# Optimization experiments

Measured on AMD Instinct MI355X. Metric: run time of the kernel, lower is better.

The kernel has to match this reference:

```python
import jax, jax.numpy as jnp
import numpy as np

V, H, O = 256, 1024, 1024   # input_dim, hidden_dim, output_dim
B, T = 64, 512


def setup_inputs() -> dict:
    key = jax.random.key(0)
    ks = jax.random.split(key, 12)
    s = 1.0 / np.sqrt(H)  # torch nn.RNN / nn.Linear init range
    u = lambda k, shp: jax.random.uniform(k, shp, jnp.float32, -s, s)
    return {
        "x": jax.random.randint(ks[0], (B, T), 0, V),
        "W_ih_f": u(ks[1], (H, V)), "W_hh_f": u(ks[2], (H, H)),
        "b_ih_f": u(ks[3], (H,)),   "b_hh_f": u(ks[4], (H,)),
        "W_ih_b": u(ks[5], (H, V)), "W_hh_b": u(ks[6], (H, H)),
        "b_ih_b": u(ks[7], (H,)),   "b_hh_b": u(ks[8], (H,)),
        "W_fc": u(ks[9], (O, 2 * H)), "b_fc": u(ks[10], (O,)),
    }


def _scan_rnn(xW, W_hh):
    # xW: [T,B,H] precomputed input contribution (x W_ih^T + b_ih + b_hh)
    def step(h, xw):
        h = jnp.tanh(xw + h @ W_hh.T)
        return h, h
    h0 = jnp.zeros((xW.shape[1], W_hh.shape[0]), xW.dtype)
    _, hs = jax.lax.scan(step, h0, xW)
    return hs  # [T,B,H]


def reference(x, W_ih_f, W_hh_f, b_ih_f, b_hh_f,
              W_ih_b, W_hh_b, b_ih_b, b_hh_b, W_fc, b_fc):
    # one_hot(x, V) @ W_ih^T  ==  W_ih.T[x]  (gather; same math, no dense one-hot)
    xW_f = W_ih_f.T[x] + b_ih_f + b_hh_f          # [B,T,H]
    xW_b = W_ih_b.T[x] + b_ih_b + b_hh_b          # [B,T,H]
    hf = _scan_rnn(jnp.swapaxes(xW_f, 0, 1), W_hh_f)            # [T,B,H]
    hb = _scan_rnn(jnp.swapaxes(xW_b, 0, 1)[::-1], W_hh_b)[::-1]  # [T,B,H]
    out = jnp.swapaxes(jnp.concatenate([hf, hb], axis=-1), 0, 1)  # [B,T,2H]
    return out @ W_fc.T + b_fc                    # [B,T,O]
```

## Files before the change

kernel.cpp:

```cpp
#include <hip/hip_runtime.h>
#include <math.h>

#define B_ 64
#define T_ 512
#define H_ 1024
#define V_ 256
#define O_ 1024
#define KFC 2048

typedef short bf16x8 __attribute__((ext_vector_type(8)));
typedef _Float16 f16x8 __attribute__((ext_vector_type(8)));
typedef float f32x4 __attribute__((ext_vector_type(4)));
typedef int   i32x4 __attribute__((ext_vector_type(4)));
typedef unsigned long long u64x2 __attribute__((ext_vector_type(2)));

#define FLIP64 0x8000800080008000ULL

#define OFF_TABLE_F 0
#define OFF_TABLE_B 1048576
#define OFF_XT      2097152
#define OFF_WHH     2228224
#define OFF_WFC     6422528
#define OFF_HSF     10616832
#define OFF_HSB     77725696

__device__ __forceinline__ float fast_tanh(float zz) {
  float e = __expf(2.0f * zz);
  return 1.0f - 2.0f * __builtin_amdgcn_rcpf(e + 1.0f);
}

__global__ void prep_kernel(const int* __restrict__ x,
    const float* __restrict__ WihF, const float* __restrict__ WhhF,
    const float* __restrict__ bihF, const float* __restrict__ bhhF,
    const float* __restrict__ WihB, const float* __restrict__ WhhB,
    const float* __restrict__ bihB, const float* __restrict__ bhhB,
    const float* __restrict__ Wfc,
    float* __restrict__ tableF, float* __restrict__ tableB,
    int* __restrict__ xT, short* __restrict__ whhpack,
    short* __restrict__ wfcpack, unsigned long long* __restrict__ hsz)
{
  const long NT1 = 524288, NT2 = 32768, NT3 = 2097152, NT4 = 2097152;
  const long NT5 = 16777216;
  const long total = NT1 + NT2 + NT3 + NT4 + NT5;
  for (long i = (long)blockIdx.x * blockDim.x + threadIdx.x; i < total;
       i += (long)gridDim.x * blockDim.x) {
    long j = i;
    if (j < NT1) {
      int d = (int)(j >> 18);
      int r = (int)(j & 262143);
      int v = r >> 10, h = r & 1023;
      const float* Wih = d ? WihB : WihF;
      const float* bi  = d ? bihB : bihF;
      const float* bh  = d ? bhhB : bhhF;
      (d ? tableB : tableF)[r] = Wih[h * V_ + v] + bi[h] + bh[h];
      continue;
    }
    j -= NT1;
    if (j < NT2) {
      int t = (int)(j >> 6), bb = (int)(j & 63);
      xT[j] = x[bb * T_ + t];
      continue;
    }
    j -= NT2;
    if (j < NT3) {
      int d = (int)(j >> 20);
      int r = (int)(j & 1048575);
      int jj = r & 7;
      int lanei = (r >> 3) & 63;
      int kt = (r >> 9) & 31;
      int cti = (r >> 14) & 3;
      int csi = (r >> 16) & 15;
      int c = csi * 64 + cti * 16 + (lanei & 15);
      int k = kt * 32 + (lanei >> 4) * 8 + jj;
      float w = (d ? WhhB : WhhF)[c * H_ + k];
      _Float16 wh = (_Float16)w;
      whhpack[j] = __builtin_bit_cast(short, wh);
      continue;
    }
    j -= NT3;
    if (j < NT4) {
      int jj = (int)(j & 7);
      int lanei = (int)((j >> 3) & 63);
      int nti = (int)((j >> 9) & 3);
      int k32 = (int)((j >> 11) & 63);
      int obi = (int)(j >> 17);
      int o = obi * 64 + nti * 16 + (lanei & 15);
      int k = k32 * 32 + (lanei >> 4) * 8 + jj;
      _Float16 wf = (_Float16)Wfc[(long)o * KFC + k];
      wfcpack[j] = __builtin_bit_cast(short, wf);
      continue;
    }
    j -= NT4;
    hsz[j] = 0ULL;
    continue;
  }
}

__global__ __launch_bounds__(256, 1)
void rnn_kernel(const int* __restrict__ xT,
                const float* __restrict__ tableF, const float* __restrict__ tableB,
                const short* __restrict__ whhpack,
                unsigned long long* __restrict__ hsfF,
                unsigned long long* __restrict__ hsfB)
{
  extern __shared__ char lds[];
  char* ldsH = lds;
  const int tid = threadIdx.x;
  const int wg = blockIdx.x;
  const int dir = wg >> 6;
  const int bt = (wg >> 4) & 3;
  const int cs = wg & 15;
  const int lane = tid & 63;
  const int ct = tid >> 6;
  const int row = bt * 16 + (lane & 15);
  const int c4 = cs * 64 + ct * 16 + (lane >> 4) * 4;
  const float* table = dir ? tableB : tableF;
  unsigned long long* hsx = dir ? hsfB : hsfF;
  const int pub_off = bt * 4096 + (c4 >> 5) * 128 + ((c4 >> 2) & 1) * 64 +
                      (lane & 15) + ((c4 >> 3) & 3) * 16;

  f16x8 Wreg[32];
  {
    const i32x4* wsrc = (const i32x4*)whhpack + (size_t)(dir * 16 + cs) * 8192;
    #pragma unroll
    for (int kt = 0; kt < 32; ++kt)
      Wreg[kt] = __builtin_bit_cast(f16x8, wsrc[(ct * 32 + kt) * 64 + lane]);
  }

  const f32x4 zv = {0.f, 0.f, 0.f, 0.f};

  {
    int t0 = dir ? 511 : 0;
    int v = xT[t0 * 64 + row];
    f32x4 xwv = *(const f32x4*)(table + v * 1024 + c4);
    unsigned long long hx = 0;
    #pragma unroll
    for (int r = 0; r < 4; ++r) {
      float h = fast_tanh(xwv[r]);
      union { _Float16 f; unsigned short u; } cv; cv.f = (_Float16)h;
      unsigned short u = (cv.u == 0x8000u) ? 0u : cv.u;
      hx |= (unsigned long long)(u ^ 0x8000u) << (16 * r);
    }
    __hip_atomic_store(hsx + (size_t)t0 * 16384 + pub_off, hx,
                       __ATOMIC_RELAXED, __HIP_MEMORY_SCOPE_AGENT);
  }

#define LDX(p) __hip_atomic_load((p), __ATOMIC_RELAXED, __HIP_MEMORY_SCOPE_AGENT)

  for (int s = 1; s < 512; ++s) {
    const int t = dir ? (511 - s) : s;
    const int tprev = dir ? (t + 1) : (t - 1);
    int v = xT[t * 64 + row];
    f32x4 xwv = *(const f32x4*)(table + v * 1024 + c4);

    const unsigned long long* sp =
        hsx + (size_t)tprev * 16384 + bt * 4096 + tid * 2;
    unsigned long long a0[4], b0[4], a1[4], b1[4];
    #pragma unroll
    for (int i = 0; i < 4; ++i) {
      a0[i] = LDX(sp + i * 512);
      b0[i] = LDX(sp + i * 512 + 1);
    }
    #pragma unroll
    for (int i = 0; i < 4; ++i) {
      a1[i] = LDX(sp + (4 + i) * 512);
      b1[i] = LDX(sp + (4 + i) * 512 + 1);
    }

    for (;;) {
      int miss = 0;
      #pragma unroll
      for (int i = 0; i < 4; ++i)
        miss |= (a0[i] == 0ULL) | (b0[i] == 0ULL);
      if (!__ballot(miss)) break;
      __builtin_amdgcn_s_sleep(1);
      #pragma unroll
      for (int i = 0; i < 4; ++i) {
        a0[i] = LDX(sp + i * 512);
        b0[i] = LDX(sp + i * 512 + 1);
      }
    }
    #pragma unroll
    for (int jj = 0; jj < 4; ++jj) {
      u64x2 w; w[0] = a0[jj] ^ FLIP64; w[1] = b0[jj] ^ FLIP64;
      *(u64x2*)(ldsH + jj * 4096 + tid * 16) = w;
    }
    asm volatile("s_waitcnt lgkmcnt(0)" ::: "memory");
    __builtin_amdgcn_s_barrier();
    asm volatile("" ::: "memory");

    f32x4 acc4[4] = {zv, zv, zv, zv};
    #pragma unroll
    for (int kt = 0; kt < 16; ++kt) {
      u64x2 bv;
      bv[0] = *(const unsigned long long*)(ldsH + (kt * 128 + lane) * 8);
      bv[1] = *(const unsigned long long*)(ldsH + (kt * 128 + 64 + lane) * 8);
      f16x8 bf = __builtin_bit_cast(f16x8, bv);
      acc4[kt & 3] =
          __builtin_amdgcn_mfma_f32_16x16x32_f16(Wreg[kt], bf, acc4[kt & 3], 0, 0, 0);
    }

    for (;;) {
      int miss = 0;
      #pragma unroll
      for (int i = 0; i < 4; ++i)
        miss |= (a1[i] == 0ULL) | (b1[i] == 0ULL);
      if (!__ballot(miss)) break;
      __builtin_amdgcn_s_sleep(1);
      #pragma unroll
      for (int i = 0; i < 4; ++i) {
        a1[i] = LDX(sp + (4 + i) * 512);
        b1[i] = LDX(sp + (4 + i) * 512 + 1);
      }
    }
    #pragma unroll
    for (int jj = 0; jj < 4; ++jj) {
      u64x2 w; w[0] = a1[jj] ^ FLIP64; w[1] = b1[jj] ^ FLIP64;
      *(u64x2*)(ldsH + (4 + jj) * 4096 + tid * 16) = w;
    }
    asm volatile("s_waitcnt lgkmcnt(0)" ::: "memory");
    __builtin_amdgcn_s_barrier();
    asm volatile("" ::: "memory");

    #pragma unroll
    for (int kt = 16; kt < 32; ++kt) {
      u64x2 bv;
      bv[0] = *(const unsigned long long*)(ldsH + (kt * 128 + lane) * 8);
      bv[1] = *(const unsigned long long*)(ldsH + (kt * 128 + 64 + lane) * 8);
      f16x8 bf = __builtin_bit_cast(f16x8, bv);
      acc4[kt & 3] =
          __builtin_amdgcn_mfma_f32_16x16x32_f16(Wreg[kt], bf, acc4[kt & 3], 0, 0, 0);
    }

    f32x4 accs = (acc4[0] + acc4[1]) + (acc4[2] + acc4[3]);
    unsigned long long hx = 0;
    #pragma unroll
    for (int r = 0; r < 4; ++r) {
      float h = fast_tanh(accs[r] + xwv[r]);
      union { _Float16 f; unsigned short u; } cv; cv.f = (_Float16)h;
      unsigned short u = (cv.u == 0x8000u) ? 0u : cv.u;
      hx |= (unsigned long long)(u ^ 0x8000u) << (16 * r);
    }
    __hip_atomic_store(hsx + (size_t)t * 16384 + pub_off, hx,
                       __ATOMIC_RELAXED, __HIP_MEMORY_SCOPE_AGENT);
  }
#undef LDX
}

__global__ __launch_bounds__(256, 2)
void fc_kernel(const unsigned long long* __restrict__ hsfF,
               const unsigned long long* __restrict__ hsfB,
               const short* __restrict__ wfcpack, const float* __restrict__ bfc,
               float* __restrict__ out)
{
  __shared__ unsigned long long Alds[4096];
  __shared__ short Blds[4096];
  const int tid = threadIdx.x;
  const int lane = tid & 63;
  const int w = tid >> 6;
  const int t = blockIdx.x * 4 + w;
  const int ob = blockIdx.y;
  const int btl = lane >> 4;
  const int li = lane & 15;

  const i32x4 flip32 = {(int)0x80008000, (int)0x80008000,
                        (int)0x80008000, (int)0x80008000};
  f32x4 z = {0.f, 0.f, 0.f, 0.f};
  f32x4 acc[4][4] = {{z, z, z, z}, {z, z, z, z}, {z, z, z, z}, {z, z, z, z}};
  unsigned long long* Aw = &Alds[w * 1024];

  for (int kc = 0; kc < 32; ++kc) {
    {
      const unsigned long long* src =
          (kc < 16 ? hsfF : hsfB) + (size_t)t * 16384;
      int kt0 = (kc & 15) * 2;
      const unsigned long long* ap = src + btl * 4096 + kt0 * 128 + li * 8;
      #pragma unroll
      for (int rr = 0; rr < 2; ++rr) {
        i32x4 q0 = *(const i32x4*)(ap + rr * 128) ^ flip32;
        i32x4 q1 = *(const i32x4*)(ap + rr * 128 + 2) ^ flip32;
        i32x4 q2 = *(const i32x4*)(ap + rr * 128 + 4) ^ flip32;
        i32x4 q3 = *(const i32x4*)(ap + rr * 128 + 6) ^ flip32;
        unsigned long long* dst = &Aw[(btl * 2 + rr) * 128 + li * 8];
        *(i32x4*)(dst) = q0;
        *(i32x4*)(dst + 2) = q1;
        *(i32x4*)(dst + 4) = q2;
        *(i32x4*)(dst + 6) = q3;
      }
    }
    {
      const i32x4* src = (const i32x4*)(wfcpack + ((size_t)ob * 64 + kc * 2) * 2048);
      i32x4* dst = (i32x4*)Blds;
      dst[tid] = src[tid];
      dst[tid + 256] = src[tid + 256];
    }
    __syncthreads();
    #pragma unroll
    for (int k2 = 0; k2 < 2; ++k2) {
      f16x8 afr[4];
      #pragma unroll
      for (int mi = 0; mi < 4; ++mi) {
        u64x2 av;
        av[0] = Aw[(mi * 2 + k2) * 128 + lane];
        av[1] = Aw[(mi * 2 + k2) * 128 + 64 + lane];
        afr[mi] = __builtin_bit_cast(f16x8, av);
      }
      #pragma unroll
      for (int ni = 0; ni < 4; ++ni) {
        f16x8 bfr = *(const f16x8*)((const char*)Blds + ((k2 * 4 + ni) * 64 + lane) * 16);
        #pragma unroll
        for (int mi = 0; mi < 4; ++mi)
          acc[mi][ni] = __builtin_amdgcn_mfma_f32_16x16x32_f16(afr[mi], bfr, acc[mi][ni], 0, 0, 0);
      }
    }
    __syncthreads();
  }
  #pragma unroll
  for (int mi = 0; mi < 4; ++mi) {
    #pragma unroll
    for (int ni = 0; ni < 4; ++ni) {
      int o = ob * 64 + ni * 16 + (lane & 15);
      float bias = bfc[o];
      #pragma unroll
      for (int r = 0; r < 4; ++r) {
        int b = mi * 16 + (lane >> 4) * 4 + r;
        out[(size_t)(b * 512 + t) * O_ + o] = acc[mi][ni][r] + bias;
      }
    }
  }
}

extern "C" void kernel_launch(void* const* d_in, const int* in_sizes, int n_in,
                              void* d_out, int out_size, void* d_ws, size_t ws_size,
                              hipStream_t stream) {
  const int* x = (const int*)d_in[0];
  const float* WihF = (const float*)d_in[1];
  const float* WhhF = (const float*)d_in[2];
  const float* bihF = (const float*)d_in[3];
  const float* bhhF = (const float*)d_in[4];
  const float* WihB = (const float*)d_in[5];
  const float* WhhB = (const float*)d_in[6];
  const float* bihB = (const float*)d_in[7];
  const float* bhhB = (const float*)d_in[8];
  const float* Wfc  = (const float*)d_in[9];
  const float* bfc  = (const float*)d_in[10];
  float* out = (float*)d_out;
  char* ws = (char*)d_ws;

  float* tableF = (float*)(ws + OFF_TABLE_F);
  float* tableB = (float*)(ws + OFF_TABLE_B);
  int* xT = (int*)(ws + OFF_XT);
  short* whhpack = (short*)(ws + OFF_WHH);
  short* wfcpack = (short*)(ws + OFF_WFC);
  unsigned long long* hsfF = (unsigned long long*)(ws + OFF_HSF);
  unsigned long long* hsfB = (unsigned long long*)(ws + OFF_HSB);

  hipFuncSetAttribute((const void*)rnn_kernel,
                      hipFuncAttributeMaxDynamicSharedMemorySize, 32768);

  prep_kernel<<<dim3(2048), dim3(256), 0, stream>>>(
      x, WihF, WhhF, bihF, bhhF, WihB, WhhB, bihB, bhhB, Wfc,
      tableF, tableB, xT, whhpack, wfcpack, hsfF);
  rnn_kernel<<<dim3(128), dim3(256), 32768, stream>>>(
      xT, tableF, tableB, whhpack, hsfF, hsfB);
  fc_kernel<<<dim3(128, 16), dim3(256), 0, stream>>>(
      hsfF, hsfB, wfcpack, bfc, out);
}
```

Baseline: 1.553 ms.

## Halve RNN workgroups, each computing two column tiles with streamed weights

The recurrent kernel now launches 64 workgroups instead of 128, and each wave computes two 16-column tiles per step instead of one. The W_hh fragments are no longer held in registers. They are reloaded from global memory (likely served from cache) inside every timestep's MFMA loop. This means fewer workgroups take part in the per-step cross-workgroup synchronisation, and register pressure drops. In exchange, each timestep now issues many global weight loads on the serial critical path and each workgroup does twice the MFMA work.

```diff
diff --git a/kernel.cpp b/kernel.cpp
--- a/kernel.cpp
+++ b/kernel.cpp
@@ -68,9 +68,8 @@
       int jj = r & 7;
       int lanei = (r >> 3) & 63;
       int kt = (r >> 9) & 31;
-      int cti = (r >> 14) & 3;
-      int csi = (r >> 16) & 15;
-      int c = csi * 64 + cti * 16 + (lanei & 15);
+      int tt = (r >> 14) & 63;
+      int c = tt * 16 + (lanei & 15);
       int k = kt * 32 + (lanei >> 4) * 8 + jj;
       float w = (d ? WhhB : WhhF)[c * H_ + k];
       _Float16 wh = (_Float16)w;
@@ -107,41 +106,44 @@
   char* ldsH = lds;
   const int tid = threadIdx.x;
   const int wg = blockIdx.x;
-  const int dir = wg >> 6;
-  const int bt = (wg >> 4) & 3;
-  const int cs = wg & 15;
+  const int dir = wg >> 5;
+  const int bt = (wg >> 3) & 3;
+  const int csh = wg & 7;
   const int lane = tid & 63;
   const int ct = tid >> 6;
+  const int tt0 = csh * 8 + ct * 2;
   const int row = bt * 16 + (lane & 15);
-  const int c4 = cs * 64 + ct * 16 + (lane >> 4) * 4;
+  const int c4a = tt0 * 16 + (lane >> 4) * 4;
+  const int c4b = c4a + 16;
   const float* table = dir ? tableB : tableF;
   unsigned long long* hsx = dir ? hsfB : hsfF;
-  const int pub_off = bt * 4096 + (c4 >> 5) * 128 + ((c4 >> 2) & 1) * 64 +
-                      (lane & 15) + ((c4 >> 3) & 3) * 16;
-
-  f16x8 Wreg[32];
-  {
-    const i32x4* wsrc = (const i32x4*)whhpack + (size_t)(dir * 16 + cs) * 8192;
-    #pragma unroll
-    for (int kt = 0; kt < 32; ++kt)
-      Wreg[kt] = __builtin_bit_cast(f16x8, wsrc[(ct * 32 + kt) * 64 + lane]);
-  }
+  const int pub_a = bt * 4096 + (c4a >> 5) * 128 + ((c4a >> 2) & 1) * 64 +
+                    (lane & 15) + ((c4a >> 3) & 3) * 16;
+  const int pub_b = pub_a + 32;
+  const i32x4* wsrc = (const i32x4*)whhpack;
+  const size_t wbase0 = (size_t)(dir * 64 + tt0) * 2048 + lane;
+  const size_t wbase1 = wbase0 + 2048;
 
   const f32x4 zv = {0.f, 0.f, 0.f, 0.f};
+
+#define ENC(h) ({ union { _Float16 f; unsigned short u; } cv_; cv_.f = (_Float16)(h); \
+                  unsigned short u_ = (cv_.u == 0x8000u) ? 0u : cv_.u; \
+                  (unsigned long long)(u_ ^ 0x8000u); })
 
   {
     int t0 = dir ? 511 : 0;
     int v = xT[t0 * 64 + row];
-    f32x4 xwv = *(const f32x4*)(table + v * 1024 + c4);
-    unsigned long long hx = 0;
+    f32x4 xwa = *(const f32x4*)(table + v * 1024 + c4a);
+    f32x4 xwb = *(const f32x4*)(table + v * 1024 + c4b);
+    unsigned long long hxa = 0, hxb = 0;
     #pragma unroll
     for (int r = 0; r < 4; ++r) {
-      float h = fast_tanh(xwv[r]);
-      union { _Float16 f; unsigned short u; } cv; cv.f = (_Float16)h;
-      unsigned short u = (cv.u == 0x8000u) ? 0u : cv.u;
-      hx |= (unsigned long long)(u ^ 0x8000u) << (16 * r);
-    }
-    __hip_atomic_store(hsx + (size_t)t0 * 16384 + pub_off, hx,
+      hxa |= ENC(fast_tanh(xwa[r])) << (16 * r);
+      hxb |= ENC(fast_tanh(xwb[r])) << (16 * r);
+    }
+    __hip_atomic_store(hsx + (size_t)t0 * 16384 + pub_a, hxa,
+                       __ATOMIC_RELAXED, __HIP_MEMORY_SCOPE_AGENT);
+    __hip_atomic_store(hsx + (size_t)t0 * 16384 + pub_b, hxb,
                        __ATOMIC_RELAXED, __HIP_MEMORY_SCOPE_AGENT);
   }
 
@@ -151,7 +153,8 @@
     const int t = dir ? (511 - s) : s;
     const int tprev = dir ? (t + 1) : (t - 1);
     int v = xT[t * 64 + row];
-    f32x4 xwv = *(const f32x4*)(table + v * 1024 + c4);
+    f32x4 xwa = *(const f32x4*)(table + v * 1024 + c4a);
+    f32x4 xwb = *(const f32x4*)(table + v * 1024 + c4b);
 
     const unsigned long long* sp =
         hsx + (size_t)tprev * 16384 + bt * 4096 + tid * 2;
@@ -189,15 +192,20 @@
     __builtin_amdgcn_s_barrier();
     asm volatile("" ::: "memory");
 
-    f32x4 acc4[4] = {zv, zv, zv, zv};
+    f32x4 accA[4] = {zv, zv, zv, zv};
+    f32x4 accB[4] = {zv, zv, zv, zv};
     #pragma unroll
     for (int kt = 0; kt < 16; ++kt) {
       u64x2 bv;
       bv[0] = *(const unsigned long long*)(ldsH + (kt * 128 + lane) * 8);
       bv[1] = *(const unsigned long long*)(ldsH + (kt * 128 + 64 + lane) * 8);
       f16x8 bf = __builtin_bit_cast(f16x8, bv);
-      acc4[kt & 3] =
-          __builtin_amdgcn_mfma_f32_16x16x32_f16(Wreg[kt], bf, acc4[kt & 3], 0, 0, 0);
+      f16x8 af0 = __builtin_bit_cast(f16x8, wsrc[wbase0 + (size_t)kt * 64]);
+      f16x8 af1 = __builtin_bit_cast(f16x8, wsrc[wbase1 + (size_t)kt * 64]);
+      accA[kt & 3] =
+          __builtin_amdgcn_mfma_f32_16x16x32_f16(af0, bf, accA[kt & 3], 0, 0, 0);
+      accB[kt & 3] =
+          __builtin_amdgcn_mfma_f32_16x16x32_f16(af1, bf, accB[kt & 3], 0, 0, 0);
     }
 
     for (;;) {
@@ -228,23 +236,29 @@
       bv[0] = *(const unsigned long long*)(ldsH + (kt * 128 + lane) * 8);
       bv[1] = *(const unsigned long long*)(ldsH + (kt * 128 + 64 + lane) * 8);
       f16x8 bf = __builtin_bit_cast(f16x8, bv);
-      acc4[kt & 3] =
-          __builtin_amdgcn_mfma_f32_16x16x32_f16(Wreg[kt], bf, acc4[kt & 3], 0, 0, 0);
-    }
-
-    f32x4 accs = (acc4[0] + acc4[1]) + (acc4[2] + acc4[3]);
-    unsigned long long hx = 0;
+      f16x8 af0 = __builtin_bit_cast(f16x8, wsrc[wbase0 + (size_t)kt * 64]);
+      f16x8 af1 = __builtin_bit_cast(f16x8, wsrc[wbase1 + (size_t)kt * 64]);
+      accA[kt & 3] =
+          __builtin_amdgcn_mfma_f32_16x16x32_f16(af0, bf, accA[kt & 3], 0, 0, 0);
+      accB[kt & 3] =
+          __builtin_amdgcn_mfma_f32_16x16x32_f16(af1, bf, accB[kt & 3], 0, 0, 0);
+    }
+
+    f32x4 accsA = (accA[0] + accA[1]) + (accA[2] + accA[3]);
+    f32x4 accsB = (accB[0] + accB[1]) + (accB[2] + accB[3]);
+    unsigned long long hxa = 0, hxb = 0;
     #pragma unroll
     for (int r = 0; r < 4; ++r) {
-      float h = fast_tanh(accs[r] + xwv[r]);
-      union { _Float16 f; unsigned short u; } cv; cv.f = (_Float16)h;
-      unsigned short u = (cv.u == 0x8000u) ? 0u : cv.u;
-      hx |= (unsigned long long)(u ^ 0x8000u) << (16 * r);
-    }
-    __hip_atomic_store(hsx + (size_t)t * 16384 + pub_off, hx,
+      hxa |= ENC(fast_tanh(accsA[r] + xwa[r])) << (16 * r);
+      hxb |= ENC(fast_tanh(accsB[r] + xwb[r])) << (16 * r);
+    }
+    __hip_atomic_store(hsx + (size_t)t * 16384 + pub_a, hxa,
                        __ATOMIC_RELAXED, __HIP_MEMORY_SCOPE_AGENT);
+    __hip_atomic_store(hsx + (size_t)t * 16384 + pub_b, hxb,
+                       __ATOMIC_RELAXED, __HIP_MEMORY_SCOPE_AGENT);
   }
 #undef LDX
+#undef ENC
 }
 
 __global__ __launch_bounds__(256, 2)
@@ -361,7 +375,7 @@
   prep_kernel<<<dim3(2048), dim3(256), 0, stream>>>(
       x, WihF, WhhF, bihF, bhhF, WihB, WhhB, bihB, bhhB, Wfc,
       tableF, tableB, xT, whhpack, wfcpack, hsfF);
-  rnn_kernel<<<dim3(128), dim3(256), 32768, stream>>>(
+  rnn_kernel<<<dim3(64), dim3(256), 32768, stream>>>(
       xT, tableF, tableB, whhpack, hsfF, hsfB);
   fc_kernel<<<dim3(128, 16), dim3(256), 0, stream>>>(
       hsfF, hsfB, wfcpack, bfc, out);
```

After: 2.360 ms. 1.52x slower.

## Fuse RNN recurrence and FC projection into one persistent kernel with overlap

Applied to the files above, without the earlier changes.

Merges the RNN and FC kernels into one launch of 256 workgroups. The first 128 run the bidirectional recurrence, and the other 128 act as FC consumers that spin-wait on the hidden-state buffers, which use zero to mean not yet written. Each FC consumer processes timesteps starting from the middle of the sequence, where both directions finish first, so the output projection overlaps the serial recurrence instead of running after it. The risks are polling traffic and contention for CUs and memory bandwidth that could slow the latency-critical recurrence. It also depends on all 256 workgroups being co-resident to avoid deadlock.

```diff
diff --git a/kernel.cpp b/kernel.cpp
--- a/kernel.cpp
+++ b/kernel.cpp
@@ -97,237 +97,255 @@
 }
 
 __global__ __launch_bounds__(256, 1)
-void rnn_kernel(const int* __restrict__ xT,
-                const float* __restrict__ tableF, const float* __restrict__ tableB,
-                const short* __restrict__ whhpack,
-                unsigned long long* __restrict__ hsfF,
-                unsigned long long* __restrict__ hsfB)
+void fused_kernel(const int* __restrict__ xT,
+                  const float* __restrict__ tableF, const float* __restrict__ tableB,
+                  const short* __restrict__ whhpack,
+                  const short* __restrict__ wfcpack, const float* __restrict__ bfc,
+                  unsigned long long* __restrict__ hsfF,
+                  unsigned long long* __restrict__ hsfB,
+                  float* __restrict__ out)
 {
   extern __shared__ char lds[];
-  char* ldsH = lds;
   const int tid = threadIdx.x;
-  const int wg = blockIdx.x;
-  const int dir = wg >> 6;
-  const int bt = (wg >> 4) & 3;
-  const int cs = wg & 15;
   const int lane = tid & 63;
-  const int ct = tid >> 6;
-  const int row = bt * 16 + (lane & 15);
-  const int c4 = cs * 64 + ct * 16 + (lane >> 4) * 4;
-  const float* table = dir ? tableB : tableF;
-  unsigned long long* hsx = dir ? hsfB : hsfF;
-  const int pub_off = bt * 4096 + (c4 >> 5) * 128 + ((c4 >> 2) & 1) * 64 +
-                      (lane & 15) + ((c4 >> 3) & 3) * 16;
-
-  f16x8 Wreg[32];
-  {
-    const i32x4* wsrc = (const i32x4*)whhpack + (size_t)(dir * 16 + cs) * 8192;
-    #pragma unroll
-    for (int kt = 0; kt < 32; ++kt)
-      Wreg[kt] = __builtin_bit_cast(f16x8, wsrc[(ct * 32 + kt) * 64 + lane]);
-  }
-
   const f32x4 zv = {0.f, 0.f, 0.f, 0.f};
 
-  {
-    int t0 = dir ? 511 : 0;
-    int v = xT[t0 * 64 + row];
-    f32x4 xwv = *(const f32x4*)(table + v * 1024 + c4);
-    unsigned long long hx = 0;
-    #pragma unroll
-    for (int r = 0; r < 4; ++r) {
-      float h = fast_tanh(xwv[r]);
-      union { _Float16 f; unsigned short u; } cv; cv.f = (_Float16)h;
-      unsigned short u = (cv.u == 0x8000u) ? 0u : cv.u;
-      hx |= (unsigned long long)(u ^ 0x8000u) << (16 * r);
-    }
-    __hip_atomic_store(hsx + (size_t)t0 * 16384 + pub_off, hx,
-                       __ATOMIC_RELAXED, __HIP_MEMORY_SCOPE_AGENT);
-  }
-
 #define LDX(p) __hip_atomic_load((p), __ATOMIC_RELAXED, __HIP_MEMORY_SCOPE_AGENT)
 
-  for (int s = 1; s < 512; ++s) {
-    const int t = dir ? (511 - s) : s;
-    const int tprev = dir ? (t + 1) : (t - 1);
-    int v = xT[t * 64 + row];
-    f32x4 xwv = *(const f32x4*)(table + v * 1024 + c4);
-
-    const unsigned long long* sp =
-        hsx + (size_t)tprev * 16384 + bt * 4096 + tid * 2;
-    unsigned long long a0[4], b0[4], a1[4], b1[4];
-    #pragma unroll
-    for (int i = 0; i < 4; ++i) {
-      a0[i] = LDX(sp + i * 512);
-      b0[i] = LDX(sp + i * 512 + 1);
-    }
-    #pragma unroll
-    for (int i = 0; i < 4; ++i) {
-      a1[i] = LDX(sp + (4 + i) * 512);
-      b1[i] = LDX(sp + (4 + i) * 512 + 1);
-    }
-
-    for (;;) {
-      int miss = 0;
-      #pragma unroll
-      for (int i = 0; i < 4; ++i)
-        miss |= (a0[i] == 0ULL) | (b0[i] == 0ULL);
-      if (!__ballot(miss)) break;
-      __builtin_amdgcn_s_sleep(1);
+  if (blockIdx.x < 128) {
+    char* ldsH = lds;
+    const int wg = blockIdx.x;
+    const int dir = wg >> 6;
+    const int bt = (wg >> 4) & 3;
+    const int cs = wg & 15;
+    const int ct = tid >> 6;
+    const int row = bt * 16 + (lane & 15);
+    const int c4 = cs * 64 + ct * 16 + (lane >> 4) * 4;
+    const float* table = dir ? tableB : tableF;
+    unsigned long long* hsx = dir ? hsfB : hsfF;
+    const int pub_off = bt * 4096 + (c4 >> 5) * 128 + ((c4 >> 2) & 1) * 64 +
+                        (lane & 15) + ((c4 >> 3) & 3) * 16;
+
+    f16x8 Wreg[32];
+    {
+      const i32x4* wsrc = (const i32x4*)whhpack + (size_t)(dir * 16 + cs) * 8192;
+      #pragma unroll
+      for (int kt = 0; kt < 32; ++kt)
+        Wreg[kt] = __builtin_bit_cast(f16x8, wsrc[(ct * 32 + kt) * 64 + lane]);
+    }
+
+    {
+      int t0 = dir ? 511 : 0;
+      int v = xT[t0 * 64 + row];
+      f32x4 xwv = *(const f32x4*)(table + v * 1024 + c4);
+      unsigned long long hx = 0;
+      #pragma unroll
+      for (int r = 0; r < 4; ++r) {
+        float h = fast_tanh(xwv[r]);
+        union { _Float16 f; unsigned short u; } cv; cv.f = (_Float16)h;
+        unsigned short u = (cv.u == 0x8000u) ? 0u : cv.u;
+        hx |= (unsigned long long)(u ^ 0x8000u) << (16 * r);
+      }
+      __hip_atomic_store(hsx + (size_t)t0 * 16384 + pub_off, hx,
+                         __ATOMIC_RELAXED, __HIP_MEMORY_SCOPE_AGENT);
+    }
+
+    for (int s = 1; s < 512; ++s) {
+      const int t = dir ? (511 - s) : s;
+      const int tprev = dir ? (t + 1) : (t - 1);
+      int v = xT[t * 64 + row];
+      f32x4 xwv = *(const f32x4*)(table + v * 1024 + c4);
+
+      const unsigned long long* sp =
+          hsx + (size_t)tprev * 16384 + bt * 4096 + tid * 2;
+      unsigned long long a0[4], b0[4], a1[4], b1[4];
       #pragma unroll
       for (int i = 0; i < 4; ++i) {
         a0[i] = LDX(sp + i * 512);
         b0[i] = LDX(sp + i * 512 + 1);
       }
-    }
-    #pragma unroll
-    for (int jj = 0; jj < 4; ++jj) {
-      u64x2 w; w[0] = a0[jj] ^ FLIP64; w[1] = b0[jj] ^ FLIP64;
-      *(u64x2*)(ldsH + jj * 4096 + tid * 16) = w;
-    }
-    asm volatile("s_waitcnt lgkmcnt(0)" ::: "memory");
-    __builtin_amdgcn_s_barrier();
-    asm volatile("" ::: "memory");
-
-    f32x4 acc4[4] = {zv, zv, zv, zv};
-    #pragma unroll
-    for (int kt = 0; kt < 16; ++kt) {
-      u64x2 bv;
-      bv[0] = *(const unsigned long long*)(ldsH + (kt * 128 + lane) * 8);
-      bv[1] = *(const unsigned long long*)(ldsH + (kt * 128 + 64 + lane) * 8);
-      f16x8 bf = __builtin_bit_cast(f16x8, bv);
-      acc4[kt & 3] =
-          __builtin_amdgcn_mfma_f32_16x16x32_f16(Wreg[kt], bf, acc4[kt & 3], 0, 0, 0);
-    }
-
-    for (;;) {
-      int miss = 0;
-      #pragma unroll
-      for (int i = 0; i < 4; ++i)
-        miss |= (a1[i] == 0ULL) | (b1[i] == 0ULL);
-      if (!__ballot(miss)) break;
-      __builtin_amdgcn_s_sleep(1);
       #pragma unroll
       for (int i = 0; i < 4; ++i) {
         a1[i] = LDX(sp + (4 + i) * 512);
         b1[i] = LDX(sp + (4 + i) * 512 + 1);
       }
-    }
-    #pragma unroll
-    for (int jj = 0; jj < 4; ++jj) {
-      u64x2 w; w[0] = a1[jj] ^ FLIP64; w[1] = b1[jj] ^ FLIP64;
-      *(u64x2*)(ldsH + (4 + jj) * 4096 + tid * 16) = w;
-    }
-    asm volatile("s_waitcnt lgkmcnt(0)" ::: "memory");
-    __builtin_amdgcn_s_barrier();
-    asm volatile("" ::: "memory");
-
-    #pragma unroll
-    for (int kt = 16; kt < 32; ++kt) {
-      u64x2 bv;
-      bv[0] = *(const unsigned long long*)(ldsH + (kt * 128 + lane) * 8);
-      bv[1] = *(const unsigned long long*)(ldsH + (kt * 128 + 64 + lane) * 8);
-      f16x8 bf = __builtin_bit_cast(f16x8, bv);
-      acc4[kt & 3] =
-          __builtin_amdgcn_mfma_f32_16x16x32_f16(Wreg[kt], bf, acc4[kt & 3], 0, 0, 0);
-    }
-
-    f32x4 accs = (acc4[0] + acc4[1]) + (acc4[2] + acc4[3]);
-    unsigned long long hx = 0;
-    #pragma unroll
-    for (int r = 0; r < 4; ++r) {
-      float h = fast_tanh(accs[r] + xwv[r]);
-      union { _Float16 f; unsigned short u; } cv; cv.f = (_Float16)h;
-      unsigned short u = (cv.u == 0x8000u) ? 0u : cv.u;
-      hx |= (unsigned long long)(u ^ 0x8000u) << (16 * r);
-    }
-    __hip_atomic_store(hsx + (size_t)t * 16384 + pub_off, hx,
-                       __ATOMIC_RELAXED, __HIP_MEMORY_SCOPE_AGENT);
+
+      for (;;) {
+        int miss = 0;
+        #pragma unroll
+        for (int i = 0; i < 4; ++i)
+          miss |= (a0[i] == 0ULL) | (b0[i] == 0ULL);
+        if (!__ballot(miss)) break;
+        __builtin_amdgcn_s_sleep(1);
+        #pragma unroll
+        for (int i = 0; i < 4; ++i) {
+          a0[i] = LDX(sp + i * 512);
+          b0[i] = LDX(sp + i * 512 + 1);
+        }
+      }
+      #pragma unroll
+      for (int jj = 0; jj < 4; ++jj) {
+        u64x2 w; w[0] = a0[jj] ^ FLIP64; w[1] = b0[jj] ^ FLIP64;
+        *(u64x2*)(ldsH + jj * 4096 + tid * 16) = w;
+      }
+      asm volatile("s_waitcnt lgkmcnt(0)" ::: "memory");
+      __builtin_amdgcn_s_barrier();
+      asm volatile("" ::: "memory");
+
+      f32x4 acc4[4] = {zv, zv, zv, zv};
+      #pragma unroll
+      for (int kt = 0; kt < 16; ++kt) {
+        u64x2 bv;
+        bv[0] = *(const unsigned long long*)(ldsH + (kt * 128 + lane) * 8);
+        bv[1] = *(const unsigned long long*)(ldsH + (kt * 128 + 64 + lane) * 8);
+        f16x8 bf = __builtin_bit_cast(f16x8, bv);
+        acc4[kt & 3] =
+            __builtin_amdgcn_mfma_f32_16x16x32_f16(Wreg[kt], bf, acc4[kt & 3], 0, 0, 0);
+      }
+
+      for (;;) {
+        int miss = 0;
+        #pragma unroll
+        for (int i = 0; i < 4; ++i)
+          miss |= (a1[i] == 0ULL) | (b1[i] == 0ULL);
+        if (!__ballot(miss)) break;
+        __builtin_amdgcn_s_sleep(1);
+        #pragma unroll
+        for (int i = 0; i < 4; ++i) {
+          a1[i] = LDX(sp + (4 + i) * 512);
+          b1[i] = LDX(sp + (4 + i) * 512 + 1);
+        }
+      }
+      #pragma unroll
+      for (int jj = 0; jj < 4; ++jj) {
+        u64x2 w; w[0] = a1[jj] ^ FLIP64; w[1] = b1[jj] ^ FLIP64;
+        *(u64x2*)(ldsH + (4 + jj) * 4096 + tid * 16) = w;
+      }
+      asm volatile("s_waitcnt lgkmcnt(0)" ::: "memory");
+      __builtin_amdgcn_s_barrier();
+      asm volatile("" ::: "memory");
+
+      #pragma unroll
+      for (int kt = 16; kt < 32; ++kt) {
+        u64x2 bv;
+        bv[0] = *(const unsigned long long*)(ldsH + (kt * 128 + lane) * 8);
+        bv[1] = *(const unsigned long long*)(ldsH + (kt * 128 + 64 + lane) * 8);
+        f16x8 bf = __builtin_bit_cast(f16x8, bv);
+        acc4[kt & 3] =
+            __builtin_amdgcn_mfma_f32_16x16x32_f16(Wreg[kt], bf, acc4[kt & 3], 0, 0, 0);
+      }
+
+      f32x4 accs = (acc4[0] + acc4[1]) + (acc4[2] + acc4[3]);
+      unsigned long long hx = 0;
+      #pragma unroll
+      for (int r = 0; r < 4; ++r) {
+        float h = fast_tanh(accs[r] + xwv[r]);
+        union { _Float16 f; unsigned short u; } cv; cv.f = (_Float16)h;
+        unsigned short u = (cv.u == 0x8000u) ? 0u : cv.u;
+        hx |= (unsigned long long)(u ^ 0x8000u) << (16 * r);
+      }
+      __hip_atomic_store(hsx + (size_t)t * 16384 + pub_off, hx,
+                         __ATOMIC_RELAXED, __HIP_MEMORY_SCOPE_AGENT);
+    }
+  } else {
+    unsigned long long* Alds = (unsigned long long*)lds;
+    short* Blds = (short*)(lds + 32768);
+    const int f = blockIdx.x - 128;
+    const int ob = f >> 3;
+    const int g8 = f & 7;
+    const int w = tid >> 6;
+    const int btl = lane >> 4;
+    const int li = lane & 15;
+    unsigned long long* Aw = &Alds[w * 1024];
+
+    for (int p = 0; p < 16; ++p) {
+      int i = p * 8 + g8;
+      int tb = (i & 1) ? (64 + (i >> 1)) : (63 - (i >> 1));
+      int t = tb * 4 + w;
+
+      {
+        const unsigned long long* sF = hsfF + (size_t)t * 16384 + lane * 256;
+        const unsigned long long* sB = hsfB + (size_t)t * 16384 + lane * 256;
+        while (__ballot((LDX(sF) == 0ULL) | (LDX(sB) == 0ULL)))
+          __builtin_amdgcn_s_sleep(32);
+      }
+
+      f32x4 acc[4][4] = {{zv, zv, zv, zv}, {zv, zv, zv, zv},
+                         {zv, zv, zv, zv}, {zv, zv, zv, zv}};
+
+      for (int kc = 0; kc < 32; ++kc) {
+        {
+          const unsigned long long* src =
+              (kc < 16 ? hsfF : hsfB) + (size_t)t * 16384;
+          int kt0 = (kc & 15) * 2;
+          const unsigned long long* ap = src + btl * 4096 + kt0 * 128 + li * 8;
+          unsigned long long vv[16];
+          #pragma unroll
+          for (int rr = 0; rr < 2; ++rr)
+            #pragma unroll
+            for (int n = 0; n < 8; ++n)
+              vv[rr * 8 + n] = LDX(ap + rr * 128 + n);
+          for (;;) {
+            int miss = 0;
+            #pragma unroll
+            for (int q = 0; q < 16; ++q) miss |= (vv[q] == 0ULL);
+            if (!__ballot(miss)) break;
+            __builtin_amdgcn_s_sleep(2);
+            #pragma unroll
+            for (int rr = 0; rr < 2; ++rr)
+              #pragma unroll
+              for (int n = 0; n < 8; ++n)
+                vv[rr * 8 + n] = LDX(ap + rr * 128 + n);
+          }
+          #pragma unroll
+          for (int rr = 0; rr < 2; ++rr)
+            #pragma unroll
+            for (int n = 0; n < 8; ++n)
+              Aw[(btl * 2 + rr) * 128 + li * 8 + n] = vv[rr * 8 + n] ^ FLIP64;
+        }
+        {
+          const i32x4* src = (const i32x4*)(wfcpack + ((size_t)ob * 64 + kc * 2) * 2048);
+          i32x4* dst = (i32x4*)Blds;
+          dst[tid] = src[tid];
+          dst[tid + 256] = src[tid + 256];
+        }
+        __syncthreads();
+        #pragma unroll
+        for (int k2 = 0; k2 < 2; ++k2) {
+          f16x8 afr[4];
+          #pragma unroll
+          for (int mi = 0; mi < 4; ++mi) {
+            u64x2 av;
+            av[0] = Aw[(mi * 2 + k2) * 128 + lane];
+            av[1] = Aw[(mi * 2 + k2) * 128 + 64 + lane];
+            afr[mi] = __builtin_bit_cast(f16x8, av);
+          }
+          #pragma unroll
+          for (int ni = 0; ni < 4; ++ni) {
+            f16x8 bfr = *(const f16x8*)((const char*)Blds + ((k2 * 4 + ni) * 64 + lane) * 16);
+            #pragma unroll
+            for (int mi = 0; mi < 4; ++mi)
+              acc[mi][ni] = __builtin_amdgcn_mfma_f32_16x16x32_f16(afr[mi], bfr, acc[mi][ni], 0, 0, 0);
+          }
+        }
+        __syncthreads();
+      }
+      #pragma unroll
+      for (int mi = 0; mi < 4; ++mi) {
+        #pragma unroll
+        for (int ni = 0; ni < 4; ++ni) {
+          int o = ob * 64 + ni * 16 + (lane & 15);
+          float bias = bfc[o];
+          #pragma unroll
+          for (int r = 0; r < 4; ++r) {
+            int b = mi * 16 + (lane >> 4) * 4 + r;
+            out[(size_t)(b * 512 + t) * O_ + o] = acc[mi][ni][r] + bias;
+          }
+        }
+      }
+    }
   }
 #undef LDX
-}
-
-__global__ __launch_bounds__(256, 2)
-void fc_kernel(const unsigned long long* __restrict__ hsfF,
-               const unsigned long long* __restrict__ hsfB,
-               const short* __restrict__ wfcpack, const float* __restrict__ bfc,
-               float* __restrict__ out)
-{
-  __shared__ unsigned long long Alds[4096];
-  __shared__ short Blds[4096];
-  const int tid = threadIdx.x;
-  const int lane = tid & 63;
-  const int w = tid >> 6;
-  const int t = blockIdx.x * 4 + w;
-  const int ob = blockIdx.y;
-  const int btl = lane >> 4;
-  const int li = lane & 15;
-
-  const i32x4 flip32 = {(int)0x80008000, (int)0x80008000,
-                        (int)0x80008000, (int)0x80008000};
-  f32x4 z = {0.f, 0.f, 0.f, 0.f};
-  f32x4 acc[4][4] = {{z, z, z, z}, {z, z, z, z}, {z, z, z, z}, {z, z, z, z}};
-  unsigned long long* Aw = &Alds[w * 1024];
-
-  for (int kc = 0; kc < 32; ++kc) {
-    {
-      const unsigned long long* src =
-          (kc < 16 ? hsfF : hsfB) + (size_t)t * 16384;
-      int kt0 = (kc & 15) * 2;
-      const unsigned long long* ap = src + btl * 4096 + kt0 * 128 + li * 8;
-      #pragma unroll
-      for (int rr = 0; rr < 2; ++rr) {
-        i32x4 q0 = *(const i32x4*)(ap + rr * 128) ^ flip32;
-        i32x4 q1 = *(const i32x4*)(ap + rr * 128 + 2) ^ flip32;
-        i32x4 q2 = *(const i32x4*)(ap + rr * 128 + 4) ^ flip32;
-        i32x4 q3 = *(const i32x4*)(ap + rr * 128 + 6) ^ flip32;
-        unsigned long long* dst = &Aw[(btl * 2 + rr) * 128 + li * 8];
-        *(i32x4*)(dst) = q0;
-        *(i32x4*)(dst + 2) = q1;
-        *(i32x4*)(dst + 4) = q2;
-        *(i32x4*)(dst + 6) = q3;
-      }
-    }
-    {
-      const i32x4* src = (const i32x4*)(wfcpack + ((size_t)ob * 64 + kc * 2) * 2048);
-      i32x4* dst = (i32x4*)Blds;
-      dst[tid] = src[tid];
-      dst[tid + 256] = src[tid + 256];
-    }
-    __syncthreads();
-    #pragma unroll
-    for (int k2 = 0; k2 < 2; ++k2) {
-      f16x8 afr[4];
-      #pragma unroll
-      for (int mi = 0; mi < 4; ++mi) {
-        u64x2 av;
-        av[0] = Aw[(mi * 2 + k2) * 128 + lane];
-        av[1] = Aw[(mi * 2 + k2) * 128 + 64 + lane];
-        afr[mi] = __builtin_bit_cast(f16x8, av);
-      }
-      #pragma unroll
-      for (int ni = 0; ni < 4; ++ni) {
-        f16x8 bfr = *(const f16x8*)((const char*)Blds + ((k2 * 4 + ni) * 64 + lane) * 16);
-        #pragma unroll
-        for (int mi = 0; mi < 4; ++mi)
-          acc[mi][ni] = __builtin_amdgcn_mfma_f32_16x16x32_f16(afr[mi], bfr, acc[mi][ni], 0, 0, 0);
-      }
-    }
-    __syncthreads();
-  }
-  #pragma unroll
-  for (int mi = 0; mi < 4; ++mi) {
-    #pragma unroll
-    for (int ni = 0; ni < 4; ++ni) {
-      int o = ob * 64 + ni * 16 + (lane & 15);
-      float bias = bfc[o];
-      #pragma unroll
-      for (int r = 0; r < 4; ++r) {
-        int b = mi * 16 + (lane >> 4) * 4 + r;
-        out[(size_t)(b * 512 + t) * O_ + o] = acc[mi][ni][r] + bias;
-      }
-    }
-  }
 }
 
 extern "C" void kernel_launch(void* const* d_in, const int* in_sizes, int n_in,
@@ -355,14 +373,12 @@
   unsigned long long* hsfF = (unsigned long long*)(ws + OFF_HSF);
   unsigned long long* hsfB = (unsigned long long*)(ws + OFF_HSB);
 
-  hipFuncSetAttribute((const void*)rnn_kernel,
-                      hipFuncAttributeMaxDynamicSharedMemorySize, 32768);
+  hipFuncSetAttribute((const void*)fused_kernel,
+                      hipFuncAttributeMaxDynamicSharedMemorySize, 40960);
 
   prep_kernel<<<dim3(2048), dim3(256), 0, stream>>>(
       x, WihF, WhhF, bihF, bhhF, WihB, WhhB, bihB, bhhB, Wfc,
       tableF, tableB, xT, whhpack, wfcpack, hsfF);
-  rnn_kernel<<<dim3(128), dim3(256), 32768, stream>>>(
-      xT, tableF, tableB, whhpack, hsfF, hsfB);
-  fc_kernel<<<dim3(128, 16), dim3(256), 0, stream>>>(
-      hsfF, hsfB, wfcpack, bfc, out);
+  fused_kernel<<<dim3(256), dim3(256), 40960, stream>>>(
+      xT, tableF, tableB, whhpack, wfcpack, bfc, hsfF, hsfB, out);
 }
```

New measurement: 2.134 ms. +37.4%, slower.

## Double FC output tile per block, swizzle A in LDS, vectorize zero-fill

Applied to the files above, without the earlier changes.

The FC kernel now computes two 64-wide output blocks per workgroup. Each loaded A tile is reused twice and the grid is halved. The A staging in LDS uses an XOR swizzle to cut bank conflicts on the fragment reads. The prep kernel zeroes the hidden-state buffers with 16-byte stores, which halves its iteration count. In exchange the accumulators double, which raises register pressure and may lower occupancy.

```diff
diff --git a/kernel.cpp b/kernel.cpp
--- a/kernel.cpp
+++ b/kernel.cpp
@@ -40,7 +40,7 @@
     short* __restrict__ wfcpack, unsigned long long* __restrict__ hsz)
 {
   const long NT1 = 524288, NT2 = 32768, NT3 = 2097152, NT4 = 2097152;
-  const long NT5 = 16777216;
+  const long NT5 = 8388608;
   const long total = NT1 + NT2 + NT3 + NT4 + NT5;
   for (long i = (long)blockIdx.x * blockDim.x + threadIdx.x; i < total;
        i += (long)gridDim.x * blockDim.x) {
@@ -91,7 +91,10 @@
       continue;
     }
     j -= NT4;
-    hsz[j] = 0ULL;
+    {
+      u64x2 zz = {0ULL, 0ULL};
+      *((u64x2*)hsz + j) = zz;
+    }
     continue;
   }
 }
@@ -254,19 +257,26 @@
                float* __restrict__ out)
 {
   __shared__ unsigned long long Alds[4096];
-  __shared__ short Blds[4096];
+  __shared__ short Blds[8192];
   const int tid = threadIdx.x;
   const int lane = tid & 63;
   const int w = tid >> 6;
   const int t = blockIdx.x * 4 + w;
-  const int ob = blockIdx.y;
+  const int ob0 = blockIdx.y * 2;
   const int btl = lane >> 4;
   const int li = lane & 15;
 
   const i32x4 flip32 = {(int)0x80008000, (int)0x80008000,
                         (int)0x80008000, (int)0x80008000};
   f32x4 z = {0.f, 0.f, 0.f, 0.f};
-  f32x4 acc[4][4] = {{z, z, z, z}, {z, z, z, z}, {z, z, z, z}, {z, z, z, z}};
+  f32x4 acc[2][4][4];
+  #pragma unroll
+  for (int ob = 0; ob < 2; ++ob)
+    #pragma unroll
+    for (int mi = 0; mi < 4; ++mi)
+      #pragma unroll
+      for (int ni = 0; ni < 4; ++ni)
+        acc[ob][mi][ni] = z;
   unsigned long long* Aw = &Alds[w * 1024];
 
   for (int kc = 0; kc < 32; ++kc) {
@@ -277,22 +287,23 @@
       const unsigned long long* ap = src + btl * 4096 + kt0 * 128 + li * 8;
       #pragma unroll
       for (int rr = 0; rr < 2; ++rr) {
-        i32x4 q0 = *(const i32x4*)(ap + rr * 128) ^ flip32;
-        i32x4 q1 = *(const i32x4*)(ap + rr * 128 + 2) ^ flip32;
-        i32x4 q2 = *(const i32x4*)(ap + rr * 128 + 4) ^ flip32;
-        i32x4 q3 = *(const i32x4*)(ap + rr * 128 + 6) ^ flip32;
-        unsigned long long* dst = &Aw[(btl * 2 + rr) * 128 + li * 8];
-        *(i32x4*)(dst) = q0;
-        *(i32x4*)(dst + 2) = q1;
-        *(i32x4*)(dst + 4) = q2;
-        *(i32x4*)(dst + 6) = q3;
+        int rowi = btl * 2 + rr;
+        const i32x4* aq = (const i32x4*)(ap + rr * 128);
+        #pragma unroll
+        for (int k = 0; k < 4; ++k) {
+          i32x4 q = aq[k] ^ flip32;
+          *(i32x4*)&Aw[rowi * 128 + (((li * 4 + k) ^ rowi) << 1)] = q;
+        }
       }
     }
     {
-      const i32x4* src = (const i32x4*)(wfcpack + ((size_t)ob * 64 + kc * 2) * 2048);
+      const i32x4* s0 = (const i32x4*)(wfcpack + ((size_t)ob0 * 64 + kc * 2) * 2048);
+      const i32x4* s1 = (const i32x4*)(wfcpack + ((size_t)(ob0 + 1) * 64 + kc * 2) * 2048);
       i32x4* dst = (i32x4*)Blds;
-      dst[tid] = src[tid];
-      dst[tid + 256] = src[tid + 256];
+      dst[tid] = s0[tid];
+      dst[tid + 256] = s0[tid + 256];
+      dst[tid + 512] = s1[tid];
+      dst[tid + 768] = s1[tid + 256];
     }
     __syncthreads();
     #pragma unroll
@@ -300,31 +311,41 @@
       f16x8 afr[4];
       #pragma unroll
       for (int mi = 0; mi < 4; ++mi) {
+        int rowi = mi * 2 + k2;
+        int s0i = ((((lane >> 1) ^ rowi) << 1)) + (lane & 1);
         u64x2 av;
-        av[0] = Aw[(mi * 2 + k2) * 128 + lane];
-        av[1] = Aw[(mi * 2 + k2) * 128 + 64 + lane];
+        av[0] = Aw[rowi * 128 + s0i];
+        av[1] = Aw[rowi * 128 + 64 + s0i];
         afr[mi] = __builtin_bit_cast(f16x8, av);
       }
       #pragma unroll
+      for (int ob = 0; ob < 2; ++ob) {
+        #pragma unroll
+        for (int ni = 0; ni < 4; ++ni) {
+          f16x8 bfr = *(const f16x8*)((const char*)Blds + ob * 8192 +
+                                      ((k2 * 4 + ni) * 64 + lane) * 16);
+          #pragma unroll
+          for (int mi = 0; mi < 4; ++mi)
+            acc[ob][mi][ni] = __builtin_amdgcn_mfma_f32_16x16x32_f16(
+                afr[mi], bfr, acc[ob][mi][ni], 0, 0, 0);
+        }
+      }
+    }
+    __syncthreads();
+  }
+  #pragma unroll
+  for (int ob = 0; ob < 2; ++ob) {
+    #pragma unroll
+    for (int mi = 0; mi < 4; ++mi) {
+      #pragma unroll
       for (int ni = 0; ni < 4; ++ni) {
-        f16x8 bfr = *(const f16x8*)((const char*)Blds + ((k2 * 4 + ni) * 64 + lane) * 16);
+        int o = (ob0 + ob) * 64 + ni * 16 + (lane & 15);
+        float bias = bfc[o];
         #pragma unroll
-        for (int mi = 0; mi < 4; ++mi)
-          acc[mi][ni] = __builtin_amdgcn_mfma_f32_16x16x32_f16(afr[mi], bfr, acc[mi][ni], 0, 0, 0);
-      }
-    }
-    __syncthreads();
-  }
-  #pragma unroll
-  for (int mi = 0; mi < 4; ++mi) {
-    #pragma unroll
-    for (int ni = 0; ni < 4; ++ni) {
-      int o = ob * 64 + ni * 16 + (lane & 15);
-      float bias = bfc[o];
-      #pragma unroll
-      for (int r = 0; r < 4; ++r) {
-        int b = mi * 16 + (lane >> 4) * 4 + r;
-        out[(size_t)(b * 512 + t) * O_ + o] = acc[mi][ni][r] + bias;
+        for (int r = 0; r < 4; ++r) {
+          int b = mi * 16 + (lane >> 4) * 4 + r;
+          out[(size_t)(b * 512 + t) * O_ + o] = acc[ob][mi][ni][r] + bias;
+        }
       }
     }
   }
@@ -363,6 +384,6 @@
       tableF, tableB, xT, whhpack, wfcpack, hsfF);
   rnn_kernel<<<dim3(128), dim3(256), 32768, stream>>>(
       xT, tableF, tableB, whhpack, hsfF, hsfB);
-  fc_kernel<<<dim3(128, 16), dim3(256), 0, stream>>>(
+  fc_kernel<<<dim3(128, 8), dim3(256), 0, stream>>>(
       hsfF, hsfB, wfcpack, bfc, out);
 }
```

Result: faster. 1.477 ms (-4.9%).
